# Kernel tuning notes

Hardware: AMD Instinct MI355X
Metric: run time of the kernel (lower is better)

The kernel has to match this reference:

```python
import jax, jax.numpy as jnp
import numpy as np

FEATURE, ENC, HEADS = 128, 64, 4


def _pe_tables(L, E):
    # PositionalEncoding: X = (1..L) / 10000**(arange(0,E,2)/E), sinx=sin(X), cosx=cos(X)
    pos = jnp.arange(1, L + 1, dtype=jnp.float32)[:, None]
    div = jnp.power(10000.0, jnp.arange(0, E, 2, dtype=jnp.float32) / E)
    X = pos / div  # (L, E/2)
    return jnp.sin(X), jnp.cos(X)


def _interleave(a, b):
    # a -> even channels, b -> odd channels
    return jnp.stack([a, b], axis=-1).reshape(a.shape[:-1] + (a.shape[-1] * 2,))


def _to_relative(X, sinx, cosx):
    s, c = X[..., 0::2], X[..., 1::2]
    return _interleave(s * cosx - c * sinx, c * cosx + s * sinx)


def _rotate(img, angle_deg, nearest=False):
    # Center rotation with zero fill on (..., H, W); bilinear (or nearest) sampling.
    H, W = img.shape[-2], img.shape[-1]
    th = float(angle_deg) * np.pi / 180.0
    co, si = float(np.cos(th)), float(np.sin(th))
    yy, xx = jnp.meshgrid(jnp.arange(H, dtype=jnp.float32), jnp.arange(W, dtype=jnp.float32), indexing='ij')
    cy, cx = (H - 1) / 2.0, (W - 1) / 2.0
    dx, dy = xx - cx, yy - cy
    sx = co * dx + si * dy + cx
    sy = -si * dx + co * dy + cy

    def gather(yi, xi):
        valid = ((yi >= 0) & (yi < H) & (xi >= 0) & (xi < W)).astype(img.dtype)
        return img[..., jnp.clip(yi, 0, H - 1), jnp.clip(xi, 0, W - 1)] * valid

    if nearest:
        return gather(jnp.round(sy).astype(jnp.int32), jnp.round(sx).astype(jnp.int32))
    x0 = jnp.floor(sx); y0 = jnp.floor(sy)
    wx = sx - x0; wy = sy - y0
    x0i, y0i = x0.astype(jnp.int32), y0.astype(jnp.int32)
    return (gather(y0i, x0i) * (1 - wy) * (1 - wx)
            + gather(y0i, x0i + 1) * (1 - wy) * wx
            + gather(y0i + 1, x0i) * wy * (1 - wx)
            + gather(y0i + 1, x0i + 1) * wy * wx)


def _att_result(mat4, mask3, Wi, bi, Wo, bo):
    # __get_attention_result: MHA(q=k=mat, v=pos_enc(zeros)), then to_relative, keep first ENC channels.
    B_, A, L, E = mat4.shape
    h, dh = HEADS, E // HEADS
    mat = mat4.reshape(-1, L, E)
    sinx, cosx = _pe_tables(L, E)
    P = _interleave(sinx, cosx)  # (L, E): pos_enc(zeros_like(mat)) is the same for every row
    q = (mat @ Wi[:E].T + bi[:E]).reshape(-1, L, h, dh)
    k = (mat @ Wi[E:2 * E].T + bi[E:2 * E]).reshape(-1, L, h, dh)
    v = (P @ Wi[2 * E:].T + bi[2 * E:]).reshape(L, h, dh)
    logits = jnp.einsum('blhd,bmhd->bhlm', q, k) / np.sqrt(dh)
    if mask3 is not None:
        # torch MHA ADDS a float key_padding_mask to the attention logits
        logits = logits + mask3.reshape(-1, L)[:, None, None, :]
    attn = jax.nn.softmax(logits, axis=-1)
    o = jnp.einsum('bhlm,mhd->blhd', attn, v).reshape(-1, L, E)
    o = o @ Wo.T + bo
    o = _to_relative(o, sinx, cosx)
    return o.reshape(B_, A, L, E)[..., :ENC]


def _forward(x, in_proj_w, in_proj_b, out_w, out_b):
    B, C, H, W = x.shape
    ph, pw = H // 2, W // 2
    p = (in_proj_w, in_proj_b, out_w, out_b)
    row_res = _att_result(x.transpose(0, 2, 3, 1), None, *p)                      # (B,H,W,ENC)
    col_res = _att_result(x.transpose(0, 3, 2, 1), None, *p).transpose(0, 2, 1, 3)
    padded = jnp.pad(x, ((0, 0), (0, 0), (ph, ph), (pw, pw)))
    mask = jnp.pad(jnp.ones((B, H, W), x.dtype), ((0, 0), (ph, ph), (pw, pw)))
    diag = []
    for ang in (45.0, -45.0):
        rx = _rotate(padded, ang).transpose(0, 2, 3, 1)                           # (B,Hp,Wp,E)
        rm = _rotate(mask, ang, nearest=True)
        r = _att_result(rx, rm, *p).transpose(0, 3, 1, 2)                         # (B,ENC,Hp,Wp)
        r = _rotate(r, -ang)[..., ph:ph + H, pw:pw + W]
        diag.append(r.transpose(0, 2, 3, 1))
    res = jnp.stack([row_res, col_res, diag[0], diag[1]], axis=-2)                # (B,H,W,4,ENC)
    res = jnp.sort(res, axis=-2).reshape(B, H, W, 4 * ENC)
    return jnp.concatenate([x, res.transpose(0, 3, 1, 2)], axis=1)                # (B, C+4*ENC, H, W)


def setup_inputs():
    key = jax.random.key(0)
    ks = jax.random.split(key, 5)
    B, H, W, E = 2, 80, 80, FEATURE
    return {
        'x': jax.random.normal(ks[0], (B, E, H, W), jnp.float32),
        'in_proj_w': jax.random.normal(ks[1], (3 * E, E), jnp.float32) * 0.05,
        'in_proj_b': jax.random.normal(ks[2], (3 * E,), jnp.float32) * 0.05,
        'out_w': jax.random.normal(ks[3], (E, E), jnp.float32) * 0.05,
        'out_b': jax.random.normal(ks[4], (E,), jnp.float32) * 0.05,
    }


def reference(x, in_proj_w, in_proj_b, out_w, out_b):
    return _forward(x, in_proj_w, in_proj_b, out_w, out_b)
```

## Files before the change

kernel.cpp:

```cpp
#include <hip/hip_runtime.h>
#include <math.h>

#ifndef M_PI
#define M_PI 3.14159265358979323846
#endif

typedef unsigned int u32;
typedef unsigned short u16;
typedef float f32x2 __attribute__((ext_vector_type(2)));
typedef short bf16x8 __attribute__((ext_vector_type(8)));
typedef float f32x16 __attribute__((ext_vector_type(16)));

#define DEVI __device__ __forceinline__
#define MFMA32(a, b, c) __builtin_amdgcn_mfma_f32_32x32x16_bf16((a), (b), (c), 0, 0, 0)

constexpr int QD    = 12800 * 128;
constexpr int Q_SZ  = 12800 * 128 + 102400 * 128;
constexpr int QC_SZ = 12800 * 128;
constexpr int RW_SZ = 2 * 2 * 160 * 160 * 64;
constexpr int RC_SZ = 2 * 80 * 80 * 64;

constexpr size_t B_S80S  = 0;
constexpr size_t B_S80C  = 20480;
constexpr size_t B_S160S = 40960;
constexpr size_t B_S160C = 81920;
constexpr size_t B_VT80  = 122880;
constexpr size_t B_VT160 = 147456;
constexpr size_t B_WO2   = 188416;
constexpr size_t B_END   = 204800;

DEVI float bf2f(u16 h) { return __uint_as_float(((u32)h) << 16); }
DEVI u16 f2bf(float f) {
    u32 u = __float_as_uint(f);
    u32 r = (u + 0x7fffu + ((u >> 16) & 1u)) >> 16;
    return (u16)r;
}
DEVI u32 pack2(float lo, float hi) { return (u32)f2bf(lo) | ((u32)f2bf(hi) << 16); }
DEVI f32x2 kpair(u32 w) {
    f32x2 r;
    r.x = __uint_as_float(w << 16);
    r.y = __uint_as_float(w & 0xffff0000u);
    return r;
}

DEVI bf16x8 mkfrag(uint2 a, uint2 b) {
    union { bf16x8 f; u32 u[4]; } z;
    z.u[0] = a.x; z.u[1] = a.y; z.u[2] = b.x; z.u[3] = b.y;
    return z.f;
}
DEVI bf16x8 mkfrag4(u32 a, u32 b, u32 c, u32 d) {
    union { bf16x8 f; u32 u[4]; } z;
    z.u[0] = a; z.u[1] = b; z.u[2] = c; z.u[3] = d;
    return z.f;
}
DEVI u32 cvtpk(float lo, float hi) {
    u32 r;
    asm("v_cvt_pk_bf16_f32 %0, %1, %2" : "=v"(r) : "v"(lo), "v"(hi));
    return r;
}

__global__ void k_tables(const float* __restrict__ Wi, const float* __restrict__ bi,
                         char* __restrict__ ws) {
    int blk = blockIdx.x, t = threadIdx.x;
    bool is80 = blk < 80;
    int l = is80 ? blk : blk - 80;
    int M = is80 ? 96 : 160;
    float* sout = (float*)(ws + (is80 ? B_S80S : B_S160S));
    float* cout = (float*)(ws + (is80 ? B_S80C : B_S160C));
    u16* vt = (u16*)(ws + (is80 ? B_VT80 : B_VT160));
    __shared__ float P[128];
    if (t < 64) {
        float dv = powf(10000.f, (float)t / 64.f);
        float X = (float)(l + 1) / dv;
        float sv = sinf(X), cv = cosf(X);
        P[2 * t] = sv; P[2 * t + 1] = cv;
        sout[l * 64 + t] = sv; cout[l * 64 + t] = cv;
    }
    __syncthreads();
    float acc = bi[256 + t];
    #pragma unroll 16
    for (int c = 0; c < 128; ++c) acc += P[c] * Wi[(256 + t) * 128 + c];
    int hh = t >> 5, d = t & 31;
    vt[(hh * 32 + d) * M + l] = f2bf(acc);
    if (!is80 && blk < 96) {
        u16* v8 = (u16*)(ws + B_VT80);
        v8[(hh * 32 + d) * 96 + blk] = 0;
    }
}

__global__ void k_wot(const float* __restrict__ Wo, u16* __restrict__ wo2) {
    int idx = blockIdx.x * 256 + threadIdx.x;
    if (idx < 64 * 128) wo2[idx] = f2bf(Wo[idx]);
}

__global__ __launch_bounds__(256) void k1_rc(const float* __restrict__ x,
                                             const float* __restrict__ Wi,
                                             const float* __restrict__ bi,
                                             u16* __restrict__ qws, u16* __restrict__ kws,
                                             u16* __restrict__ qcol, u16* __restrict__ kcol) {
    __shared__ float matS[80][17];
    __shared__ float wS[256][17];
    int t = threadIdx.x;
    int blk = blockIdx.x;
    int b = blk / 80, a = blk % 80;
    int pg = t & 15, jg = t >> 4;
    float acc[5][16];
    #pragma unroll
    for (int jj = 0; jj < 16; ++jj) {
        float bv = bi[jg * 16 + jj];
        #pragma unroll
        for (int pp = 0; pp < 5; ++pp) acc[pp][jj] = bv;
    }
    for (int c0 = 0; c0 < 128; c0 += 16) {
        for (int idx = t; idx < 80 * 16; idx += 256) {
            int l = idx % 80, cc = idx / 80;
            matS[l][cc] = x[(b * 128 + c0 + cc) * 6400 + a * 80 + l];
        }
        {
            const float* wrow = Wi + t * 128 + c0;
            #pragma unroll
            for (int cc = 0; cc < 16; ++cc) wS[t][cc] = wrow[cc];
        }
        __syncthreads();
        #pragma unroll 4
        for (int cc = 0; cc < 16; ++cc) {
            float m[5];
            #pragma unroll
            for (int pp = 0; pp < 5; ++pp) m[pp] = matS[pg * 5 + pp][cc];
            #pragma unroll
            for (int jj = 0; jj < 16; ++jj) {
                float wv = wS[jg * 16 + jj][cc];
                #pragma unroll
                for (int pp = 0; pp < 5; ++pp) acc[pp][jj] += m[pp] * wv;
            }
        }
        __syncthreads();
    }
    int j0 = jg * 16;
    bool isQ = (j0 < 128);
    float sc = isQ ? 0.17677669529663687f : 1.0f;
    u16* baser = isQ ? qws : kws;
    u16* basec = isQ ? qcol : kcol;
    int jb = isQ ? j0 : (j0 - 128);
    #pragma unroll
    for (int pp = 0; pp < 5; ++pp) {
        int p = pg * 5 + pp;
        size_t pixr = (size_t)(b * 80 + a) * 80 + p;
        size_t pixc = (size_t)(b * 80 + p) * 80 + a;
        u32 wv[8];
        #pragma unroll
        for (int i = 0; i < 8; ++i) wv[i] = pack2(acc[pp][2 * i] * sc, acc[pp][2 * i + 1] * sc);
        u32* dr = (u32*)(baser + pixr * 128 + jb);
        u32* dc = (u32*)(basec + pixc * 128 + jb);
        #pragma unroll
        for (int i = 0; i < 8; ++i) { dr[i] = wv[i]; dc[i] = wv[i]; }
    }
}

__global__ __launch_bounds__(256) void k1_interp(const float* __restrict__ bi,
                                                 u16* __restrict__ qws, u16* __restrict__ kws,
                                                 float co, float si) {
    int t = threadIdx.x;
    int c = t & 63;
    int w = t >> 6;
    int W = blockIdx.x * 4 + w;
    const float sc = 0.17677669529663687f;
    f32x2 bq = {bi[2 * c] * sc, bi[2 * c + 1] * sc};
    f32x2 bk = {bi[128 + 2 * c], bi[128 + 2 * c + 1]};
    const u32* qsrc = (const u32*)qws;
    const u32* ksrc = (const u32*)kws;
    u32* qdst = (u32*)qws + (size_t)QD / 2;
    u32* kdst = (u32*)kws + (size_t)QD / 2;

    #pragma unroll 2
    for (int i = 0; i < 10; ++i) {
        int pix = W * 10 + i;
        int seqd = pix / 160;
        int p = pix % 160;
        int rot = seqd / 320;
        int a = seqd % 160;
        int b = (seqd / 160) & 1;
        float sir = rot ? -si : si;
        float dxx = (float)p - 79.5f, dyy = (float)a - 79.5f;
        float sx = co * dxx + sir * dyy + 79.5f;
        float sy = -sir * dxx + co * dyy + 79.5f;
        float x0f = floorf(sx), y0f = floorf(sy);
        int x0 = (int)x0f, y0 = (int)y0f;
        float wx = sx - x0f, wy = sy - y0f;
        float wt[4] = {(1.f - wy) * (1.f - wx), (1.f - wy) * wx, wy * (1.f - wx), wy * wx};
        int ty[4] = {y0, y0, y0 + 1, y0 + 1};
        int tx[4] = {x0, x0 + 1, x0, x0 + 1};
        f32x2 qa = {0.f, 0.f}, ka = {0.f, 0.f};
        float wsum = 0.f;
        #pragma unroll
        for (int k = 0; k < 4; ++k) {
            int yy = ty[k], xx = tx[k];
            if (yy >= 40 && yy < 120 && xx >= 40 && xx < 120) {
                size_t src = ((size_t)(b * 80 + (yy - 40)) * 80 + (xx - 40)) * 64 + c;
                f32x2 wv = {wt[k], wt[k]};
                qa += wv * kpair(qsrc[src]);
                ka += wv * kpair(ksrc[src]);
                wsum += wt[k];
            }
        }
        float rem = 1.f - wsum;
        f32x2 rem2 = {rem, rem};
        qa += rem2 * bq;
        ka += rem2 * bk;
        size_t dst = (size_t)(seqd * 160 + p) * 64 + c;
        qdst[dst] = pack2(qa.x, qa.y);
        kdst[dst] = pack2(ka.x, ka.y);
    }
}

template <int V>
DEVI void att_body(const char* __restrict__ ws, const float* __restrict__ bo,
                   float co, float si, int qp, int seq,
                   u16* __restrict__ oS, float* __restrict__ biasS) {
    constexpr int L  = V ? 160 : 80;
    constexpr int MT = V ? 5 : 3;
    constexpr int KC = V ? 10 : 6;
    int t = threadIdx.x;
    int lane = t & 63;
    int w = t >> 6;
    int hh = __builtin_amdgcn_readfirstlane(w);
    int g = lane >> 5;
    int ln31 = lane & 31;

    const u16* qws  = (const u16*)(ws + B_END);
    const u16* kws  = qws + Q_SZ;
    const u16* qcol = kws + Q_SZ;
    const u16* kcol = qcol + QC_SZ;
    u16* rws    = (u16*)(ws + B_END) + (size_t)Q_SZ * 2 + (size_t)QC_SZ * 2;
    u16* rowres = rws + RW_SZ;
    u16* colres = rowres + RC_SZ;

    int b = 0, a = 0, isCol = 0, rot = 0, seqd = 0;
    const u16 *qb, *kb;
    if (V == 1) {
        rot = seq / 320;
        int r = seq % 320;
        b = r / 160; a = r % 160;
        seqd = (rot * 2 + b) * 160 + a;
        qb = qws + (size_t)QD + (size_t)seqd * 160 * 128;
        kb = kws + (size_t)QD + (size_t)seqd * 160 * 128;
    } else {
        isCol = (seq >= 160) ? 1 : 0;
        int r = seq - isCol * 160;
        b = r / 80; a = r % 80;
        size_t base = (size_t)(b * 80 + a) * 80 * 128;
        qb = (isCol ? qcol : qws) + base;
        kb = (isCol ? kcol : kws) + base;
    }

    if (V == 1) {
        float sir = rot ? -si : si;
        float dyy = (float)a - 79.5f;
        if (t < 160) {
            float dxm = (float)t - 79.5f;
            float sx = co * dxm + sir * dyy + 79.5f;
            float sy = -sir * dxm + co * dyy + 79.5f;
            int xi = (int)rintf(sx), yi = (int)rintf(sy);
            biasS[t] = (xi >= 40 && xi < 120 && yi >= 40 && yi < 120) ? 1.0f : 0.0f;
        }
        __syncthreads();
    }
    float bfr[MT];
    #pragma unroll
    for (int mt = 0; mt < MT; ++mt) {
        if (V == 1) bfr[mt] = biasS[ln31 + 32 * mt];
        else bfr[mt] = (mt == 2) ? ((ln31 + 64 < 80) ? 0.f : -30000.f) : 0.f;
    }
    bf16x8 onef = mkfrag4((g == 0) ? 0x3F80u : 0u, 0u, 0u, 0u);

    const u16* vt = (const u16*)(ws + (V ? B_VT160 : B_VT80));
    constexpr int M = V ? 160 : 96;
    const u16* vhead = vt + (size_t)hh * 32 * M;

    #pragma unroll
    for (int sub = 0; sub < 2; ++sub) {
        int c0 = qp * 64 + sub * 32;
        if (c0 >= L) continue;
        int l = c0 + ln31;
        int lq = (l < L) ? l : (L - 1);
        const u16* qr = qb + (size_t)lq * 128 + hh * 32;
        bf16x8 qf0 = mkfrag(*(const uint2*)(qr + 4 * g), *(const uint2*)(qr + 8 + 4 * g));
        bf16x8 qf1 = mkfrag(*(const uint2*)(qr + 16 + 4 * g), *(const uint2*)(qr + 24 + 4 * g));

        f32x16 acc[MT];
        #pragma unroll
        for (int mt = 0; mt < MT; ++mt)
            #pragma unroll
            for (int r = 0; r < 16; ++r) acc[mt][r] = 0.f;

        #pragma unroll
        for (int mt = 0; mt < MT; ++mt) {
            int mrow = 32 * mt + ln31;
            if (mrow > L - 1) mrow = L - 1;
            const u16* kr = kb + (size_t)mrow * 128 + hh * 32;
            bf16x8 k0 = mkfrag(*(const uint2*)(kr + 4 * g), *(const uint2*)(kr + 8 + 4 * g));
            bf16x8 k1 = mkfrag(*(const uint2*)(kr + 16 + 4 * g), *(const uint2*)(kr + 24 + 4 * g));
            acc[mt] = MFMA32(k0, qf0, acc[mt]);
            acc[mt] = MFMA32(k1, qf1, acc[mt]);
            if (V == 1 || mt == 2) {
                u32 ab = (g == 0) ? (u32)f2bf(bfr[mt]) : 0u;
                acc[mt] = MFMA32(mkfrag4(ab, 0u, 0u, 0u), onef, acc[mt]);
            }
        }

        float mx = -3.0e38f;
        #pragma unroll
        for (int mt = 0; mt < MT; ++mt)
            #pragma unroll
            for (int r = 0; r < 16; ++r) mx = fmaxf(mx, acc[mt][r]);
        mx = fmaxf(mx, __shfl_xor(mx, 32));
        float ssum = 0.f;
        #pragma unroll
        for (int mt = 0; mt < MT; ++mt)
            #pragma unroll
            for (int r = 0; r < 16; ++r) {
                float e = __expf(acc[mt][r] - mx);
                acc[mt][r] = e;
                ssum += e;
            }
        ssum += __shfl_xor(ssum, 32);
        float inv = __builtin_amdgcn_rcpf(ssum);
        #pragma unroll
        for (int mt = 0; mt < MT; ++mt)
            #pragma unroll
            for (int r = 0; r < 16; ++r) acc[mt][r] *= inv;

        f32x16 O;
        #pragma unroll
        for (int r = 0; r < 16; ++r) O[r] = 0.f;
        #pragma unroll
        for (int kc = 0; kc < KC; ++kc) {
            int mt = kc >> 1, hb = (kc & 1) * 8;
            bf16x8 pa;
            {
                union { bf16x8 f; u32 u[4]; } z;
                z.u[0] = cvtpk(acc[mt][hb + 0], acc[mt][hb + 1]);
                z.u[1] = cvtpk(acc[mt][hb + 2], acc[mt][hb + 3]);
                z.u[2] = cvtpk(acc[mt][hb + 4], acc[mt][hb + 5]);
                z.u[3] = cvtpk(acc[mt][hb + 6], acc[mt][hb + 7]);
                pa = z.f;
            }
            const u16* vr = vhead + (size_t)ln31 * M + kc * 16 + 4 * g;
            bf16x8 vf = mkfrag(*(const uint2*)vr, *(const uint2*)(vr + 8));
            O = MFMA32(pa, vf, O);
        }

        #pragma unroll
        for (int r = 0; r < 16; ++r) {
            int row = sub * 32 + (r & 3) + 8 * (r >> 2) + 4 * g;
            u32 byteoff = (u32)(row * 256 + (hh * 32 + ln31) * 2) ^ (u32)((row & 7) << 4);
            *(u16*)((char*)oS + byteoff) = f2bf(O[r]);
        }
    }
    __syncthreads();

    int lt = w >> 1, et = w & 1;
    int e = et * 32 + ln31;
    int arow = lt * 32 + ln31;
    const u16* wo2 = (const u16*)(ws + B_WO2);
    f32x16 C;
    #pragma unroll
    for (int r = 0; r < 16; ++r) C[r] = 0.f;
    #pragma unroll
    for (int kc = 0; kc < 8; ++kc) {
        u32 ba = (u32)(arow * 256 + kc * 32 + 8 * g) ^ (u32)((arow & 7) << 4);
        u32 bb = (u32)(arow * 256 + kc * 32 + 8 * g + 16) ^ (u32)((arow & 7) << 4);
        bf16x8 af = mkfrag(*(const uint2*)((const char*)oS + ba),
                           *(const uint2*)((const char*)oS + bb));
        const u16* wr = wo2 + (size_t)e * 128 + kc * 16 + 4 * g;
        bf16x8 wf = mkfrag(*(const uint2*)wr, *(const uint2*)(wr + 8));
        C = MFMA32(af, wf, C);
    }
    float boe = bo[e];
    const float* sT = (const float*)(ws + (V ? B_S160S : B_S80S));
    const float* cT = (const float*)(ws + (V ? B_S160C : B_S80C));
    #pragma unroll
    for (int r = 0; r < 16; ++r) {
        int lg = qp * 64 + lt * 32 + (r & 3) + 8 * (r >> 2) + 4 * g;
        int lgc = (lg < L) ? lg : (L - 1);
        float v = C[r] + boe;
        float sn = sT[lgc * 64 + (e >> 1)], cs = cT[lgc * 64 + (e >> 1)];
        float part = __shfl_xor(v, 1);
        float res = (e & 1) ? (v * cs + part * sn) : (v * cs - part * sn);
        if (lg < L) {
            u16* dst;
            if (V == 1) dst = rws + (size_t)(seqd * 160 + lg) * 64;
            else if (isCol) dst = colres + (size_t)((b * 80 + lg) * 80 + a) * 64;
            else dst = rowres + (size_t)((b * 80 + a) * 80 + lg) * 64;
            dst[e] = f2bf(res);
        }
    }
}

__global__ __launch_bounds__(256, 2) void k_att_mfma(const char* __restrict__ ws,
                                                     const float* __restrict__ bo,
                                                     float co, float si) {
    __shared__ __align__(16) u16 oS[64 * 128];
    __shared__ float biasS[160];
    int flat = blockIdx.x;
    if (flat < 1920) {
        att_body<1>(ws, bo, co, si, flat / 640, flat % 640, oS, biasS);
    } else {
        int r = flat - 1920;
        att_body<0>(ws, bo, co, si, r / 320, r % 320, oS, biasS);
    }
}

__global__ __launch_bounds__(256) void k3(const u16* __restrict__ rowres,
                                          const u16* __restrict__ colres,
                                          const u16* __restrict__ rws,
                                          float* __restrict__ out, float co, float si) {
    __shared__ float buf[40][257];
    int t = threadIdx.x;
    int blk = blockIdx.x;
    int b = blk / 160;
    int rem = blk % 160;
    int h = rem >> 1;
    int half = rem & 1;
    int w0 = half * 40;
    int e = t & 63, wv = t >> 6;
    for (int k = 0; k < 10; ++k) {
        int wl = wv * 10 + k;
        int w = w0 + wl;
        size_t pix = (size_t)(b * 80 + h) * 80 + w;
        float v0 = bf2f(rowres[pix * 64 + e]);
        float v1 = bf2f(colres[pix * 64 + e]);
        float dxx = (float)(w + 40) - 79.5f, dyy = (float)(h + 40) - 79.5f;
        float dvals[2];
        #pragma unroll
        for (int r = 0; r < 2; ++r) {
            float sirb = r ? si : -si;
            float sx = co * dxx + sirb * dyy + 79.5f;
            float sy = -sirb * dxx + co * dyy + 79.5f;
            float x0 = floorf(sx), y0 = floorf(sy);
            int xi = (int)x0, yi = (int)y0;
            float wx = sx - x0, wy = sy - y0;
            const u16* rb = rws + (size_t)((r * 2 + b) * 160) * 160 * 64;
            float t00 = (yi >= 0 && yi < 160 && xi >= 0 && xi < 160) ? bf2f(rb[((size_t)yi * 160 + xi) * 64 + e]) : 0.f;
            float t01 = (yi >= 0 && yi < 160 && xi + 1 >= 0 && xi + 1 < 160) ? bf2f(rb[((size_t)yi * 160 + xi + 1) * 64 + e]) : 0.f;
            float t10 = (yi + 1 >= 0 && yi + 1 < 160 && xi >= 0 && xi < 160) ? bf2f(rb[((size_t)(yi + 1) * 160 + xi) * 64 + e]) : 0.f;
            float t11 = (yi + 1 >= 0 && yi + 1 < 160 && xi + 1 >= 0 && xi + 1 < 160) ? bf2f(rb[((size_t)(yi + 1) * 160 + xi + 1) * 64 + e]) : 0.f;
            dvals[r] = (1.f - wy) * ((1.f - wx) * t00 + wx * t01) + wy * ((1.f - wx) * t10 + wx * t11);
        }
        float a0 = v0, a1 = v1, a2 = dvals[0], a3 = dvals[1];
        float mn, mx;
        mn = fminf(a0, a1); mx = fmaxf(a0, a1); a0 = mn; a1 = mx;
        mn = fminf(a2, a3); mx = fmaxf(a2, a3); a2 = mn; a3 = mx;
        mn = fminf(a0, a2); mx = fmaxf(a0, a2); a0 = mn; a2 = mx;
        mn = fminf(a1, a3); mx = fmaxf(a1, a3); a1 = mn; a3 = mx;
        mn = fminf(a1, a2); mx = fmaxf(a1, a2); a1 = mn; a2 = mx;
        buf[wl][0 * 64 + e] = a0;
        buf[wl][1 * 64 + e] = a1;
        buf[wl][2 * 64 + e] = a2;
        buf[wl][3 * 64 + e] = a3;
    }
    __syncthreads();
    for (int idx = t; idx < 256 * 40; idx += 256) {
        int c = idx / 40, wl = idx % 40;
        out[(size_t)((b * 384 + 128 + c) * 80 + h) * 80 + w0 + wl] = buf[wl][c];
    }
}

__global__ void k_copy(const float* __restrict__ x, float* __restrict__ out) {
    int idx = blockIdx.x * 256 + threadIdx.x;
    if (idx < 409600) {
        float4 v = ((const float4*)x)[idx];
        int b = idx / 204800;
        int rem = idx % 204800;
        ((float4*)out)[(size_t)b * 614400 + rem] = v;
    }
}

extern "C" void kernel_launch(void* const* d_in, const int* in_sizes, int n_in,
                              void* d_out, int out_size, void* d_ws, size_t ws_size,
                              hipStream_t stream) {
    (void)in_sizes; (void)n_in; (void)out_size;
    const float* x  = (const float*)d_in[0];
    const float* Wi = (const float*)d_in[1];
    const float* bi = (const float*)d_in[2];
    const float* Wo = (const float*)d_in[3];
    const float* bo = (const float*)d_in[4];
    float* out = (float*)d_out;

    char* ws = (char*)d_ws;
    u16* wo2  = (u16*)(ws + B_WO2);
    u16* qws  = (u16*)(ws + B_END);
    u16* kws  = qws + Q_SZ;
    u16* qcol = kws + Q_SZ;
    u16* kcol = qcol + QC_SZ;
    u16* rws  = kcol + QC_SZ;
    u16* rowres = rws + RW_SZ;
    u16* colres = rowres + RC_SZ;

    size_t need = B_END + ((size_t)Q_SZ * 2 + (size_t)QC_SZ * 2 + RW_SZ + (size_t)RC_SZ * 2) * 2;
    if (ws_size < need) return;

    double th = 45.0 * M_PI / 180.0;
    float co = (float)cos(th), si = (float)sin(th);

    k_tables<<<dim3(240), dim3(128), 0, stream>>>(Wi, bi, ws);
    k_wot<<<dim3(32), dim3(256), 0, stream>>>(Wo, wo2);
    k1_rc<<<dim3(160), dim3(256), 0, stream>>>(x, Wi, bi, qws, kws, qcol, kcol);
    k1_interp<<<dim3(2560), dim3(256), 0, stream>>>(bi, qws, kws, co, si);
    k_att_mfma<<<dim3(2560), dim3(256), 0, stream>>>(ws, bo, co, si);
    k3<<<dim3(320), dim3(256), 0, stream>>>(rowres, colres, rws, out, co, si);
    k_copy<<<dim3(1600), dim3(256), 0, stream>>>(x, out);
}
```

Measured before the change: 256.1 us.

## Pre-swizzle Q/K/V/Wo into MFMA fragment-major layouts for coalesced loads

The interpolation kernel now stages rotated Q/K rows in shared memory and writes them out in a fragment-tiled layout. The attention kernel can then load each MFMA operand as four coalesced dword loads instead of strided 8-byte row loads. The V table and the out-projection weights are stored in the same fragment-major form, and the LDS swizzle for the output tile is changed. In exchange, the interpolation kernel gains an extra shared-memory transpose and a barrier, and the index arithmetic becomes more complex.

```diff
diff --git a/kernel.cpp b/kernel.cpp
--- a/kernel.cpp
+++ b/kernel.cpp
@@ -14,11 +14,21 @@
 #define DEVI __device__ __forceinline__
 #define MFMA32(a, b, c) __builtin_amdgcn_mfma_f32_32x32x16_bf16((a), (b), (c), 0, 0, 0)
 
-constexpr int QD    = 12800 * 128;
-constexpr int Q_SZ  = 12800 * 128 + 102400 * 128;
-constexpr int QC_SZ = 12800 * 128;
-constexpr int RW_SZ = 2 * 2 * 160 * 160 * 64;
-constexpr int RC_SZ = 2 * 80 * 80 * 64;
+constexpr int    QR_SZ   = 12800 * 128;
+constexpr size_t QTD_U32 = (size_t)640 * 5 * 2048;
+constexpr int    RW_SZ   = 2 * 2 * 160 * 160 * 64;
+constexpr int    RC_SZ   = 2 * 80 * 80 * 64;
+
+constexpr size_t O_QWS  = 0;
+constexpr size_t O_KWS  = QR_SZ;
+constexpr size_t O_QCOL = 2 * (size_t)QR_SZ;
+constexpr size_t O_KCOL = 3 * (size_t)QR_SZ;
+constexpr size_t O_QTD  = 4 * (size_t)QR_SZ;
+constexpr size_t O_KTD  = O_QTD + 2 * QTD_U32;
+constexpr size_t O_RWS  = O_KTD + 2 * QTD_U32;
+constexpr size_t O_ROW  = O_RWS + RW_SZ;
+constexpr size_t O_COL  = O_ROW + RC_SZ;
+constexpr size_t O_END  = O_COL + RC_SZ;
 
 constexpr size_t B_S80S  = 0;
 constexpr size_t B_S80C  = 20480;
@@ -42,7 +52,6 @@
     r.y = __uint_as_float(w & 0xffff0000u);
     return r;
 }
-
 DEVI bf16x8 mkfrag(uint2 a, uint2 b) {
     union { bf16x8 f; u32 u[4]; } z;
     z.u[0] = a.x; z.u[1] = a.y; z.u[2] = b.x; z.u[3] = b.y;
@@ -58,16 +67,17 @@
     asm("v_cvt_pk_bf16_f32 %0, %1, %2" : "=v"(r) : "v"(lo), "v"(hi));
     return r;
 }
+
 
 __global__ void k_tables(const float* __restrict__ Wi, const float* __restrict__ bi,
                          char* __restrict__ ws) {
     int blk = blockIdx.x, t = threadIdx.x;
     bool is80 = blk < 80;
     int l = is80 ? blk : blk - 80;
-    int M = is80 ? 96 : 160;
+    int KC = is80 ? 6 : 10;
     float* sout = (float*)(ws + (is80 ? B_S80S : B_S160S));
     float* cout = (float*)(ws + (is80 ? B_S80C : B_S160C));
-    u16* vt = (u16*)(ws + (is80 ? B_VT80 : B_VT160));
+    u32* vt = (u32*)(ws + (is80 ? B_VT80 : B_VT160));
     __shared__ float P[128];
     if (t < 64) {
         float dv = powf(10000.f, (float)t / 64.f);
@@ -81,16 +91,33 @@
     #pragma unroll 16
     for (int c = 0; c < 128; ++c) acc += P[c] * Wi[(256 + t) * 128 + c];
     int hh = t >> 5, d = t & 31;
-    vt[(hh * 32 + d) * M + l] = f2bf(acc);
+    {
+        int m = l, kc = m >> 4, o16 = m & 15;
+        int g = (o16 >> 2) & 1, jl = (o16 >> 1) & 1, hi = o16 >> 3, half = o16 & 1;
+        int S = hi * 4 + jl * 2 + g;
+        ((u16*)(vt + ((size_t)(hh * KC + kc) * 8 + S) * 32 + d))[half] = f2bf(acc);
+    }
     if (!is80 && blk < 96) {
-        u16* v8 = (u16*)(ws + B_VT80);
-        v8[(hh * 32 + d) * 96 + blk] = 0;
-    }
-}
-
-__global__ void k_wot(const float* __restrict__ Wo, u16* __restrict__ wo2) {
+        u32* v8 = (u32*)(ws + B_VT80);
+        int m = blk, kc = m >> 4, o16 = m & 15;
+        int g = (o16 >> 2) & 1, jl = (o16 >> 1) & 1, hi = o16 >> 3, half = o16 & 1;
+        int S = hi * 4 + jl * 2 + g;
+        ((u16*)(v8 + ((size_t)(hh * 6 + kc) * 8 + S) * 32 + d))[half] = 0;
+    }
+}
+
+__global__ void k_wot(const float* __restrict__ Wo, u32* __restrict__ wt) {
     int idx = blockIdx.x * 256 + threadIdx.x;
-    if (idx < 64 * 128) wo2[idx] = f2bf(Wo[idx]);
+    if (idx < 64 * 64) {
+        int e = idx >> 6, p = idx & 63;
+        int ch = 2 * p;
+        int kc = ch >> 4, o16 = ch & 15;
+        int g = (o16 >> 2) & 1, jl = (o16 >> 1) & 1, hi = o16 >> 3;
+        int S = hi * 4 + jl * 2 + g;
+        int et = e >> 5, lane = e & 31;
+        wt[((size_t)(et * 8 + kc) * 8 + S) * 32 + lane] =
+            pack2(Wo[e * 128 + ch], Wo[e * 128 + ch + 1]);
+    }
 }
 
 __global__ __launch_bounds__(256) void k1_rc(const float* __restrict__ x,
@@ -158,30 +185,32 @@
 }
 
 __global__ __launch_bounds__(256) void k1_interp(const float* __restrict__ bi,
-                                                 u16* __restrict__ qws, u16* __restrict__ kws,
+                                                 const u16* __restrict__ qws,
+                                                 const u16* __restrict__ kws,
+                                                 u32* __restrict__ qtd, u32* __restrict__ ktd,
                                                  float co, float si) {
+    __shared__ u32 qS[32][65];
+    __shared__ u32 kS[32][65];
     int t = threadIdx.x;
     int c = t & 63;
     int w = t >> 6;
-    int W = blockIdx.x * 4 + w;
+    int bid = blockIdx.x;
+    int seqd = bid / 5, chunk = bid % 5;
+    int rot = seqd / 320;
+    int a = seqd % 160;
+    int b = (seqd / 160) & 1;
+    float sir = rot ? -si : si;
     const float sc = 0.17677669529663687f;
     f32x2 bq = {bi[2 * c] * sc, bi[2 * c + 1] * sc};
     f32x2 bk = {bi[128 + 2 * c], bi[128 + 2 * c + 1]};
     const u32* qsrc = (const u32*)qws;
     const u32* ksrc = (const u32*)kws;
-    u32* qdst = (u32*)qws + (size_t)QD / 2;
-    u32* kdst = (u32*)kws + (size_t)QD / 2;
-
-    #pragma unroll 2
-    for (int i = 0; i < 10; ++i) {
-        int pix = W * 10 + i;
-        int seqd = pix / 160;
-        int p = pix % 160;
-        int rot = seqd / 320;
-        int a = seqd % 160;
-        int b = (seqd / 160) & 1;
-        float sir = rot ? -si : si;
-        float dxx = (float)p - 79.5f, dyy = (float)a - 79.5f;
+    float dyy = (float)a - 79.5f;
+
+    for (int i = 0; i < 8; ++i) {
+        int lp = w * 8 + i;
+        int p = chunk * 32 + lp;
+        float dxx = (float)p - 79.5f;
         float sx = co * dxx + sir * dyy + 79.5f;
         float sy = -sir * dxx + co * dyy + 79.5f;
         float x0f = floorf(sx), y0f = floorf(sy);
@@ -207,9 +236,24 @@
         f32x2 rem2 = {rem, rem};
         qa += rem2 * bq;
         ka += rem2 * bk;
-        size_t dst = (size_t)(seqd * 160 + p) * 64 + c;
-        qdst[dst] = pack2(qa.x, qa.y);
-        kdst[dst] = pack2(ka.x, ka.y);
+        qS[lp][c] = pack2(qa.x, qa.y);
+        kS[lp][c] = pack2(ka.x, ka.y);
+    }
+    __syncthreads();
+    size_t tbase = (size_t)bid * 2048;
+    int lane = t & 31;
+    #pragma unroll
+    for (int it = 0; it < 16; ++it) {
+        int scol = it * 8 + (t >> 5);
+        int field = scol >> 6;
+        int head = (scol >> 4) & 3;
+        int S16 = scol & 15;
+        int fr = S16 >> 3, s = S16 & 7;
+        int g = s & 1, jl = (s >> 1) & 1, hi = s >> 2;
+        int p2 = head * 16 + fr * 8 + hi * 4 + g * 2 + jl;
+        u32 v = field ? kS[lane][p2] : qS[lane][p2];
+        u32* dst = (field ? ktd : qtd) + tbase + (size_t)(head * 16 + S16) * 32 + lane;
+        *dst = v;
     }
 }
 
@@ -227,23 +271,24 @@
     int g = lane >> 5;
     int ln31 = lane & 31;
 
-    const u16* qws  = (const u16*)(ws + B_END);
-    const u16* kws  = qws + Q_SZ;
-    const u16* qcol = kws + Q_SZ;
-    const u16* kcol = qcol + QC_SZ;
-    u16* rws    = (u16*)(ws + B_END) + (size_t)Q_SZ * 2 + (size_t)QC_SZ * 2;
-    u16* rowres = rws + RW_SZ;
-    u16* colres = rowres + RC_SZ;
+    const u16* wsb  = (const u16*)(ws + B_END);
+    const u16* qws  = wsb + O_QWS;
+    const u16* kws  = wsb + O_KWS;
+    const u16* qcol = wsb + O_QCOL;
+    const u16* kcol = wsb + O_KCOL;
+    const u32* qtd  = (const u32*)(wsb + O_QTD);
+    const u32* ktd  = (const u32*)(wsb + O_KTD);
+    u16* rws    = (u16*)(wsb + O_RWS);
+    u16* rowres = (u16*)(wsb + O_ROW);
+    u16* colres = (u16*)(wsb + O_COL);
 
     int b = 0, a = 0, isCol = 0, rot = 0, seqd = 0;
-    const u16 *qb, *kb;
+    const u16 *qb = nullptr, *kb = nullptr;
     if (V == 1) {
         rot = seq / 320;
         int r = seq % 320;
         b = r / 160; a = r % 160;
         seqd = (rot * 2 + b) * 160 + a;
-        qb = qws + (size_t)QD + (size_t)seqd * 160 * 128;
-        kb = kws + (size_t)QD + (size_t)seqd * 160 * 128;
     } else {
         isCol = (seq >= 160) ? 1 : 0;
         int r = seq - isCol * 160;
@@ -273,19 +318,25 @@
     }
     bf16x8 onef = mkfrag4((g == 0) ? 0x3F80u : 0u, 0u, 0u, 0u);
 
-    const u16* vt = (const u16*)(ws + (V ? B_VT160 : B_VT80));
-    constexpr int M = V ? 160 : 96;
-    const u16* vhead = vt + (size_t)hh * 32 * M;
+    const u32* vt32 = (const u32*)(ws + (V ? B_VT160 : B_VT80));
+    const u32* vhead = vt32 + (size_t)hh * KC * 256;
 
     #pragma unroll
     for (int sub = 0; sub < 2; ++sub) {
         int c0 = qp * 64 + sub * 32;
         if (c0 >= L) continue;
-        int l = c0 + ln31;
-        int lq = (l < L) ? l : (L - 1);
-        const u16* qr = qb + (size_t)lq * 128 + hh * 32;
-        bf16x8 qf0 = mkfrag(*(const uint2*)(qr + 4 * g), *(const uint2*)(qr + 8 + 4 * g));
-        bf16x8 qf1 = mkfrag(*(const uint2*)(qr + 16 + 4 * g), *(const uint2*)(qr + 24 + 4 * g));
+        bf16x8 qf0, qf1;
+        if (V == 1) {
+            const u32* qtb = qtd + (size_t)(seqd * 5 + (qp * 2 + sub)) * 2048 + (size_t)hh * 512;
+            qf0 = mkfrag4(qtb[lane], qtb[64 + lane], qtb[128 + lane], qtb[192 + lane]);
+            qf1 = mkfrag4(qtb[256 + lane], qtb[320 + lane], qtb[384 + lane], qtb[448 + lane]);
+        } else {
+            int l = c0 + ln31;
+            int lq = (l < L) ? l : (L - 1);
+            const u16* qr = qb + (size_t)lq * 128 + hh * 32;
+            qf0 = mkfrag(*(const uint2*)(qr + 4 * g), *(const uint2*)(qr + 8 + 4 * g));
+            qf1 = mkfrag(*(const uint2*)(qr + 16 + 4 * g), *(const uint2*)(qr + 24 + 4 * g));
+        }
 
         f32x16 acc[MT];
         #pragma unroll
@@ -295,11 +346,18 @@
 
         #pragma unroll
         for (int mt = 0; mt < MT; ++mt) {
-            int mrow = 32 * mt + ln31;
-            if (mrow > L - 1) mrow = L - 1;
-            const u16* kr = kb + (size_t)mrow * 128 + hh * 32;
-            bf16x8 k0 = mkfrag(*(const uint2*)(kr + 4 * g), *(const uint2*)(kr + 8 + 4 * g));
-            bf16x8 k1 = mkfrag(*(const uint2*)(kr + 16 + 4 * g), *(const uint2*)(kr + 24 + 4 * g));
+            bf16x8 k0, k1;
+            if (V == 1) {
+                const u32* ktb = ktd + (size_t)(seqd * 5 + mt) * 2048 + (size_t)hh * 512;
+                k0 = mkfrag4(ktb[lane], ktb[64 + lane], ktb[128 + lane], ktb[192 + lane]);
+                k1 = mkfrag4(ktb[256 + lane], ktb[320 + lane], ktb[384 + lane], ktb[448 + lane]);
+            } else {
+                int mrow = 32 * mt + ln31;
+                if (mrow > L - 1) mrow = L - 1;
+                const u16* kr = kb + (size_t)mrow * 128 + hh * 32;
+                k0 = mkfrag(*(const uint2*)(kr + 4 * g), *(const uint2*)(kr + 8 + 4 * g));
+                k1 = mkfrag(*(const uint2*)(kr + 16 + 4 * g), *(const uint2*)(kr + 24 + 4 * g));
+            }
             acc[mt] = MFMA32(k0, qf0, acc[mt]);
             acc[mt] = MFMA32(k1, qf1, acc[mt]);
             if (V == 1 || mt == 2) {
@@ -345,15 +403,15 @@
                 z.u[3] = cvtpk(acc[mt][hb + 6], acc[mt][hb + 7]);
                 pa = z.f;
             }
-            const u16* vr = vhead + (size_t)ln31 * M + kc * 16 + 4 * g;
-            bf16x8 vf = mkfrag(*(const uint2*)vr, *(const uint2*)(vr + 8));
+            const u32* vtb = vhead + (size_t)kc * 256;
+            bf16x8 vf = mkfrag4(vtb[lane], vtb[64 + lane], vtb[128 + lane], vtb[192 + lane]);
             O = MFMA32(pa, vf, O);
         }
 
         #pragma unroll
         for (int r = 0; r < 16; ++r) {
             int row = sub * 32 + (r & 3) + 8 * (r >> 2) + 4 * g;
-            u32 byteoff = (u32)(row * 256 + (hh * 32 + ln31) * 2) ^ (u32)((row & 7) << 4);
+            u32 byteoff = ((u32)(row * 256 + (hh * 32 + ln31) * 2)) ^ ((u32)(row & 15) << 3);
             *(u16*)((char*)oS + byteoff) = f2bf(O[r]);
         }
     }
@@ -362,18 +420,19 @@
     int lt = w >> 1, et = w & 1;
     int e = et * 32 + ln31;
     int arow = lt * 32 + ln31;
-    const u16* wo2 = (const u16*)(ws + B_WO2);
+    const u32* wt32 = (const u32*)(ws + B_WO2);
     f32x16 C;
     #pragma unroll
     for (int r = 0; r < 16; ++r) C[r] = 0.f;
     #pragma unroll
     for (int kc = 0; kc < 8; ++kc) {
-        u32 ba = (u32)(arow * 256 + kc * 32 + 8 * g) ^ (u32)((arow & 7) << 4);
-        u32 bb = (u32)(arow * 256 + kc * 32 + 8 * g + 16) ^ (u32)((arow & 7) << 4);
+        u32 xsw = (u32)(arow & 15) << 3;
+        u32 ba = ((u32)(arow * 256 + kc * 32 + 8 * g)) ^ xsw;
+        u32 bb = ((u32)(arow * 256 + kc * 32 + 8 * g + 16)) ^ xsw;
         bf16x8 af = mkfrag(*(const uint2*)((const char*)oS + ba),
                            *(const uint2*)((const char*)oS + bb));
-        const u16* wr = wo2 + (size_t)e * 128 + kc * 16 + 4 * g;
-        bf16x8 wf = mkfrag(*(const uint2*)wr, *(const uint2*)(wr + 8));
+        const u32* wtb = wt32 + (size_t)(et * 8 + kc) * 256;
+        bf16x8 wf = mkfrag4(wtb[lane], wtb[64 + lane], wtb[128 + lane], wtb[192 + lane]);
         C = MFMA32(af, wf, C);
     }
     float boe = bo[e];
@@ -488,25 +547,28 @@
     float* out = (float*)d_out;
 
     char* ws = (char*)d_ws;
-    u16* wo2  = (u16*)(ws + B_WO2);
-    u16* qws  = (u16*)(ws + B_END);
-    u16* kws  = qws + Q_SZ;
-    u16* qcol = kws + Q_SZ;
-    u16* kcol = qcol + QC_SZ;
-    u16* rws  = kcol + QC_SZ;
-    u16* rowres = rws + RW_SZ;
-    u16* colres = rowres + RC_SZ;
-
-    size_t need = B_END + ((size_t)Q_SZ * 2 + (size_t)QC_SZ * 2 + RW_SZ + (size_t)RC_SZ * 2) * 2;
+    u32* wt   = (u32*)(ws + B_WO2);
+    u16* wsb  = (u16*)(ws + B_END);
+    u16* qws  = wsb + O_QWS;
+    u16* kws  = wsb + O_KWS;
+    u16* qcol = wsb + O_QCOL;
+    u16* kcol = wsb + O_KCOL;
+    u32* qtd  = (u32*)(wsb + O_QTD);
+    u32* ktd  = (u32*)(wsb + O_KTD);
+    u16* rowres = wsb + O_ROW;
+    u16* colres = wsb + O_COL;
+    u16* rws    = wsb + O_RWS;
+
+    size_t need = B_END + O_END * 2;
     if (ws_size < need) return;
 
     double th = 45.0 * M_PI / 180.0;
     float co = (float)cos(th), si = (float)sin(th);
 
     k_tables<<<dim3(240), dim3(128), 0, stream>>>(Wi, bi, ws);
-    k_wot<<<dim3(32), dim3(256), 0, stream>>>(Wo, wo2);
+    k_wot<<<dim3(16), dim3(256), 0, stream>>>(Wo, wt);
     k1_rc<<<dim3(160), dim3(256), 0, stream>>>(x, Wi, bi, qws, kws, qcol, kcol);
-    k1_interp<<<dim3(2560), dim3(256), 0, stream>>>(bi, qws, kws, co, si);
+    k1_interp<<<dim3(3200), dim3(256), 0, stream>>>(bi, qws, kws, qtd, ktd, co, si);
     k_att_mfma<<<dim3(2560), dim3(256), 0, stream>>>(ws, bo, co, si);
     k3<<<dim3(320), dim3(256), 0, stream>>>(rowres, colres, rws, out, co, si);
     k_copy<<<dim3(1600), dim3(256), 0, stream>>>(x, out);
```

Measured after the change: 226.3 us. 11.6% less time.
